# Kernel tuning notes

Measured on AMD Instinct MI355X. Metric: run time of the kernel, lower is better.

Reference implementation:

```python
import jax, jax.numpy as jnp
import numpy as np

T, D, H, E, A = 4096, 1024, 2048, 8, 2


def setup_inputs() -> dict:
    key = jax.random.key(0)
    k1, k2, k3, k4, k5 = jax.random.split(key, 5)
    x = jax.random.normal(k1, (T, D), dtype=jnp.float32)
    expert_indices = jax.random.randint(k2, (T, A), 0, E, dtype=jnp.int64)
    scale = 0.02  # keep activations numerically sane (torch.randn init is unscaled)
    w_gate = jax.random.normal(k3, (E, H, D), dtype=jnp.float32) * scale
    w_up = jax.random.normal(k4, (E, H, D), dtype=jnp.float32) * scale
    w_down = jax.random.normal(k5, (E, D, H), dtype=jnp.float32) * scale
    return {"x": x, "expert_indices": expert_indices,
            "w_gate": w_gate, "w_up": w_up, "w_down": w_down}


def reference(x, expert_indices, w_gate, w_up, w_down):
    # Math identical to: gather per-token expert weights then einsum, but
    # computed as dense all-expert GEMMs + small activation gathers so we
    # never materialize the (T, A, H, D) gathered weight tensors.
    zg = jnp.einsum('td,ehd->teh', x, w_gate)   # (T, E, H)
    zu = jnp.einsum('td,ehd->teh', x, w_up)     # (T, E, H)
    idx = expert_indices[:, :, None]            # (T, A, 1)
    g = jnp.take_along_axis(zg, idx, axis=1)    # (T, A, H)
    u = jnp.take_along_axis(zu, idx, axis=1)    # (T, A, H)
    h = jax.nn.silu(g) * u                      # (T, A, H)
    # Down projection: route h back to its expert with one-hot, dense GEMM.
    oh = jax.nn.one_hot(expert_indices, E, dtype=h.dtype)  # (T, A, E)
    he = jnp.einsum('tah,tae->taeh', h, oh)     # (T, A, E, H)
    out = jnp.einsum('taeh,edh->tad', he, w_down)  # (T, A, D)
    return out
```

## Files before the change

kernel.cpp:

```cpp
#include <hip/hip_runtime.h>

#define NE 8
#define TA 8192
#define MAXT 40
#define MAXPAD (MAXT*256)

typedef __attribute__((ext_vector_type(4)))  float f32x4;
typedef __attribute__((ext_vector_type(16))) float f32x16;
typedef __attribute__((ext_vector_type(8)))  short s16x8;

#define WS_CNT  0
#define WS_CUR  8
#define WS_META 16
#define WS_TEXP 18
#define WS_PERM 256

#define WAITVM0() asm volatile("s_waitcnt vmcnt(0)" ::: "memory")
#define BAR()     asm volatile("s_barrier" ::: "memory")

__device__ __forceinline__ unsigned short f2bf(float f) {
  unsigned u = __builtin_bit_cast(unsigned, f);
  u += 0x7FFFu + ((u >> 16) & 1u);
  return (unsigned short)(u >> 16);
}

__device__ __forceinline__ void glds16(const unsigned short* g, unsigned short* l) {
  __builtin_amdgcn_global_load_lds(
      (const __attribute__((address_space(1))) unsigned int*)g,
      (__attribute__((address_space(3))) unsigned int*)l, 16, 0, 0);
}

template <int STRIDE>
__device__ __forceinline__ void stage_t(const unsigned short* g, unsigned short* Lb,
                                        int k0, int tid) {
#pragma unroll
  for (int i = 0; i < 4; ++i)
    glds16(g + (size_t)i * 64 * STRIDE + k0, Lb + i * 4096 + tid * 8);
}

__global__ void k_count(const int* __restrict__ idx, int* __restrict__ ws) {
  int i = blockIdx.x * 256 + threadIdx.x;
  if (i < TA) atomicAdd(&ws[WS_CNT + idx[i]], 1);
}

__global__ void k_scan(int* __restrict__ ws) {
  if (threadIdx.x == 0) {
    int off = 0, ti = 0;
    for (int e = 0; e < NE; ++e) {
      ws[WS_CUR + e] = off;
      int c = ws[WS_CNT + e];
      int nt = (c + 255) / 256;
      for (int k = 0; k < nt; ++k) ws[WS_TEXP + ti++] = e;
      off += nt * 256;
    }
    ws[WS_META] = ti;
    ws[WS_META + 1] = off;
  }
}

__global__ void k_place(const int* __restrict__ idx, int* __restrict__ ws) {
  int i = blockIdx.x * 256 + threadIdx.x;
  if (i < TA) {
    int e = idx[i];
    int pos = atomicAdd(&ws[WS_CUR + e], 1);
    ws[WS_PERM + pos] = i;
  }
}

__global__ void k_cvt(const float* __restrict__ s, unsigned short* __restrict__ d) {
  int i = (blockIdx.x * 256 + threadIdx.x) * 8;
  f32x4 a = *(const f32x4*)(s + i);
  f32x4 b = *(const f32x4*)(s + i + 4);
  s16x8 o;
  o[0] = (short)f2bf(a[0]); o[1] = (short)f2bf(a[1]);
  o[2] = (short)f2bf(a[2]); o[3] = (short)f2bf(a[3]);
  o[4] = (short)f2bf(b[0]); o[5] = (short)f2bf(b[1]);
  o[6] = (short)f2bf(b[2]); o[7] = (short)f2bf(b[3]);
  *(s16x8*)(d + i) = o;
}

__global__ void k_cvt_gu(const float* __restrict__ s, unsigned short* __restrict__ d, int off) {
  int t = blockIdx.x * 256 + threadIdx.x;
  int i = t * 8;
  int dd = i & 1023;
  int h = (i >> 10) & 2047;
  int e = i >> 21;
  int drow = (e << 12) + ((h >> 5) << 6) + off + (h & 31);
  f32x4 a = *(const f32x4*)(s + i);
  f32x4 b = *(const f32x4*)(s + i + 4);
  s16x8 o;
  o[0] = (short)f2bf(a[0]); o[1] = (short)f2bf(a[1]);
  o[2] = (short)f2bf(a[2]); o[3] = (short)f2bf(a[3]);
  o[4] = (short)f2bf(b[0]); o[5] = (short)f2bf(b[1]);
  o[6] = (short)f2bf(b[2]); o[7] = (short)f2bf(b[3]);
  *(s16x8*)(d + (size_t)drow * 1024 + dd) = o;
}

__global__ void k_gather(const float* __restrict__ x, const int* __restrict__ ws,
                         unsigned short* __restrict__ xb) {
  int tid = blockIdx.x * 256 + threadIdx.x;
  int r = tid >> 7;
  int c = (tid & 127) << 3;
  int ta = ws[WS_PERM + r];
  s16x8 o = {0,0,0,0,0,0,0,0};
  if (ta >= 0) {
    const float* xp = x + (size_t)(ta >> 1) * 1024 + c;
    f32x4 a = *(const f32x4*)xp;
    f32x4 b = *(const f32x4*)(xp + 4);
    o[0] = (short)f2bf(a[0]); o[1] = (short)f2bf(a[1]);
    o[2] = (short)f2bf(a[2]); o[3] = (short)f2bf(a[3]);
    o[4] = (short)f2bf(b[0]); o[5] = (short)f2bf(b[1]);
    o[6] = (short)f2bf(b[2]); o[7] = (short)f2bf(b[3]);
  }
  *(s16x8*)(xb + (size_t)r * 1024 + c) = o;
}

__global__ __launch_bounds__(512) void k_gemm1(
    const unsigned short* __restrict__ xb, const unsigned short* __restrict__ wgu,
    unsigned short* __restrict__ hb, const int* __restrict__ ws) {
  int mt = blockIdx.y;
  if (mt >= ws[WS_META]) return;
  int e = ws[WS_TEXP + mt];
  int nt = blockIdx.x;

  __shared__ unsigned short L[2][32768];

  int tid = threadIdx.x;
  int lane = tid & 63, wid = tid >> 6;
  int wm = wid >> 2, wn = wid & 3;
  int lr = tid >> 3;
  int cs = (tid & 7) ^ (lr & 7);

  const unsigned short* gA = xb  + (size_t)(mt * 256 + lr) * 1024 + cs * 8;
  const unsigned short* gB = wgu + (size_t)(e * 4096 + nt * 256 + lr) * 1024 + cs * 8;

  f32x16 accg[4] = {};
  f32x16 accu[4] = {};

  int r31 = lane & 31, kg = lane >> 5, x7 = r31 & 7;
  int arow = wm * 128 + r31;
  int brow = wn * 64 + r31;

  stage_t<1024>(gA, &L[0][0], 0, tid);
  stage_t<1024>(gB, &L[0][16384], 0, tid);

#pragma unroll 2
  for (int kt = 0; kt < 16; ++kt) {
    int cur = kt & 1;
    WAITVM0();
    BAR();
    if (kt + 1 < 16) {
      stage_t<1024>(gA, &L[cur ^ 1][0],     (kt + 1) * 64, tid);
      stage_t<1024>(gB, &L[cur ^ 1][16384], (kt + 1) * 64, tid);
    }
    const unsigned short* Ab = &L[cur][0];
    const unsigned short* Bb = &L[cur][16384];
#pragma unroll
    for (int ks = 0; ks < 4; ++ks) {
      int kc = ks * 2 + kg;
      int slot = (kc ^ x7) * 8;
      s16x8 a[4], bg, bu;
#pragma unroll
      for (int mi = 0; mi < 4; ++mi)
        a[mi] = *(const s16x8*)&Ab[(arow + mi * 32) * 64 + slot];
      bg = *(const s16x8*)&Bb[brow * 64 + slot];
      bu = *(const s16x8*)&Bb[(brow + 32) * 64 + slot];
      __builtin_amdgcn_s_setprio(1);
#pragma unroll
      for (int mi = 0; mi < 4; ++mi) {
        accg[mi] = __builtin_amdgcn_mfma_f32_32x32x16_bf16(a[mi], bg, accg[mi], 0, 0, 0);
        accu[mi] = __builtin_amdgcn_mfma_f32_32x32x16_bf16(a[mi], bu, accu[mi], 0, 0, 0);
      }
      __builtin_amdgcn_s_setprio(0);
    }
  }

  int hrow0 = mt * 256 + wm * 128;
  int hcol  = nt * 128 + wn * 32 + r31;
#pragma unroll
  for (int mi = 0; mi < 4; ++mi)
#pragma unroll
    for (int r = 0; r < 16; ++r) {
      int crow = (r & 3) + 8 * (r >> 2) + 4 * kg;
      float g = accg[mi][r];
      float u = accu[mi][r];
      float h = (g / (1.f + __expf(-g))) * u;
      hb[(size_t)(hrow0 + mi * 32 + crow) * 2048 + hcol] = f2bf(h);
    }
}

__global__ __launch_bounds__(512) void k_gemm2(
    const unsigned short* __restrict__ hb, const unsigned short* __restrict__ wdb,
    float* __restrict__ out, const int* __restrict__ ws) {
  int mt = blockIdx.y;
  if (mt >= ws[WS_META]) return;
  int e = ws[WS_TEXP + mt];
  int nt = blockIdx.x;

  __shared__ unsigned short L[2][32768];

  int tid = threadIdx.x;
  int lane = tid & 63, wid = tid >> 6;
  int wm = wid >> 2, wn = wid & 3;
  int lr = tid >> 3;
  int cs = (tid & 7) ^ (lr & 7);

  const unsigned short* gA = hb  + (size_t)(mt * 256 + lr) * 2048 + cs * 8;
  const unsigned short* gB = wdb + (size_t)(e * 1024 + nt * 256 + lr) * 2048 + cs * 8;

  f32x16 acc0[4] = {};
  f32x16 acc1[4] = {};

  int r31 = lane & 31, kg = lane >> 5, x7 = r31 & 7;
  int arow = wm * 128 + r31;
  int brow = wn * 64 + r31;

  stage_t<2048>(gA, &L[0][0], 0, tid);
  stage_t<2048>(gB, &L[0][16384], 0, tid);

#pragma unroll 2
  for (int kt = 0; kt < 32; ++kt) {
    int cur = kt & 1;
    WAITVM0();
    BAR();
    if (kt + 1 < 32) {
      stage_t<2048>(gA, &L[cur ^ 1][0],     (kt + 1) * 64, tid);
      stage_t<2048>(gB, &L[cur ^ 1][16384], (kt + 1) * 64, tid);
    }
    const unsigned short* Ab = &L[cur][0];
    const unsigned short* Bb = &L[cur][16384];
#pragma unroll
    for (int ks = 0; ks < 4; ++ks) {
      int kc = ks * 2 + kg;
      int slot = (kc ^ x7) * 8;
      s16x8 a[4], b0, b1;
#pragma unroll
      for (int mi = 0; mi < 4; ++mi)
        a[mi] = *(const s16x8*)&Ab[(arow + mi * 32) * 64 + slot];
      b0 = *(const s16x8*)&Bb[brow * 64 + slot];
      b1 = *(const s16x8*)&Bb[(brow + 32) * 64 + slot];
      __builtin_amdgcn_s_setprio(1);
#pragma unroll
      for (int mi = 0; mi < 4; ++mi) {
        acc0[mi] = __builtin_amdgcn_mfma_f32_32x32x16_bf16(a[mi], b0, acc0[mi], 0, 0, 0);
        acc1[mi] = __builtin_amdgcn_mfma_f32_32x32x16_bf16(a[mi], b1, acc1[mi], 0, 0, 0);
      }
      __builtin_amdgcn_s_setprio(0);
    }
  }

  int prow0 = mt * 256 + wm * 128;
  int dcol  = nt * 256 + wn * 64 + r31;
#pragma unroll
  for (int mi = 0; mi < 4; ++mi)
#pragma unroll
    for (int r = 0; r < 16; ++r) {
      int crow = (r & 3) + 8 * (r >> 2) + 4 * kg;
      int ta = ws[WS_PERM + prow0 + mi * 32 + crow];
      if (ta >= 0) {
        out[(size_t)ta * 1024 + dcol]      = acc0[mi][r];
        out[(size_t)ta * 1024 + dcol + 32] = acc1[mi][r];
      }
    }
}

extern "C" void kernel_launch(void* const* d_in, const int* in_sizes, int n_in,
                              void* d_out, int out_size, void* d_ws, size_t ws_size,
                              hipStream_t stream) {
  const float* x   = (const float*)d_in[0];
  const int*   idx = (const int*)d_in[1];
  const float* wg  = (const float*)d_in[2];
  const float* wu  = (const float*)d_in[3];
  const float* wd  = (const float*)d_in[4];
  float* out = (float*)d_out;

  int*  wsi = (int*)d_ws;
  char* wsb = (char*)d_ws;
  const size_t OFF_XB  = 65536;
  const size_t OFF_WDB = 65536;
  const size_t OFF_WGU = 65536 + (size_t)NE * 1024 * 2048 * 2;
  const size_t OFF_HB  = OFF_WGU + (size_t)NE * 4096 * 1024 * 2;
  unsigned short* xbuf = (unsigned short*)(wsb + OFF_XB);
  unsigned short* wdb  = (unsigned short*)(wsb + OFF_WDB);
  unsigned short* wgu  = (unsigned short*)(wsb + OFF_WGU);
  unsigned short* hb   = (unsigned short*)(wsb + OFF_HB);

  hipMemsetAsync(wsi, 0, 96 * sizeof(int), stream);
  hipMemsetAsync(wsi + WS_PERM, 0xFF, MAXPAD * sizeof(int), stream);

  k_count<<<TA / 256, 256, 0, stream>>>(idx, wsi);
  k_scan<<<1, 64, 0, stream>>>(wsi);
  k_place<<<TA / 256, 256, 0, stream>>>(idx, wsi);

  k_cvt_gu<<<(NE * 2048 * 1024) / (256 * 8), 256, 0, stream>>>(wg, wgu, 0);
  k_cvt_gu<<<(NE * 2048 * 1024) / (256 * 8), 256, 0, stream>>>(wu, wgu, 32);
  k_gather<<<(MAXPAD * 128) / 256, 256, 0, stream>>>(x, wsi, xbuf);

  k_gemm1<<<dim3(16, MAXT), 512, 0, stream>>>(xbuf, wgu, hb, wsi);

  k_cvt<<<(NE * 1024 * 2048) / (256 * 8), 256, 0, stream>>>(wd, wdb);

  k_gemm2<<<dim3(4, MAXT), 512, 0, stream>>>(hb, wdb, out, wsi);
}
```

Before: 317.6 us.

## Fuse routing kernels, merge gate/up conversion, finer-grained pipelining, split-K down GEMM

Replaces the count/scan/place kernels and two memsets with a single-block routing kernel using shared-memory counters. Gate and up weight conversion is merged into one kernel. Both GEMMs now stage K in 32-wide halves with partial vmcnt waits, so the next tile's loads overlap compute at finer granularity. The down GEMM is split in two along K, with atomic float adds into a zeroed output, which doubles its block count at the cost of atomic traffic and a memset.

```diff
diff --git a/kernel.cpp b/kernel.cpp
--- a/kernel.cpp
+++ b/kernel.cpp
@@ -9,13 +9,12 @@
 typedef __attribute__((ext_vector_type(16))) float f32x16;
 typedef __attribute__((ext_vector_type(8)))  short s16x8;
 
-#define WS_CNT  0
 #define WS_CUR  8
 #define WS_META 16
 #define WS_TEXP 18
 #define WS_PERM 256
 
-#define WAITVM0() asm volatile("s_waitcnt vmcnt(0)" ::: "memory")
+#define WAITVM(N) asm volatile("s_waitcnt vmcnt(" #N ")" ::: "memory")
 #define BAR()     asm volatile("s_barrier" ::: "memory")
 
 __device__ __forceinline__ unsigned short f2bf(float f) {
@@ -30,41 +29,60 @@
       (__attribute__((address_space(3))) unsigned int*)l, 16, 0, 0);
 }
 
-template <int STRIDE>
-__device__ __forceinline__ void stage_t(const unsigned short* g, unsigned short* Lb,
-                                        int k0, int tid) {
-#pragma unroll
-  for (int i = 0; i < 4; ++i)
-    glds16(g + (size_t)i * 64 * STRIDE + k0, Lb + i * 4096 + tid * 8);
-}
-
-__global__ void k_count(const int* __restrict__ idx, int* __restrict__ ws) {
-  int i = blockIdx.x * 256 + threadIdx.x;
-  if (i < TA) atomicAdd(&ws[WS_CNT + idx[i]], 1);
-}
-
-__global__ void k_scan(int* __restrict__ ws) {
-  if (threadIdx.x == 0) {
+__global__ void k_route(const int* __restrict__ idx, int* __restrict__ ws) {
+  __shared__ int cnt[NE];
+  int t = threadIdx.x;
+  if (t < NE) cnt[t] = 0;
+  __syncthreads();
+  int e0[8];
+#pragma unroll
+  for (int k = 0; k < 8; ++k) { e0[k] = idx[t + k * 1024]; atomicAdd(&cnt[e0[k]], 1); }
+  __syncthreads();
+  if (t == 0) {
     int off = 0, ti = 0;
     for (int e = 0; e < NE; ++e) {
       ws[WS_CUR + e] = off;
-      int c = ws[WS_CNT + e];
-      int nt = (c + 255) / 256;
-      for (int k = 0; k < nt; ++k) ws[WS_TEXP + ti++] = e;
-      off += nt * 256;
+      int c = cnt[e];
+      int ntl = (c + 255) >> 8;
+      for (int k = 0; k < ntl; ++k) ws[WS_TEXP + ti++] = e;
+      off += ntl << 8;
     }
     ws[WS_META] = ti;
     ws[WS_META + 1] = off;
   }
-}
-
-__global__ void k_place(const int* __restrict__ idx, int* __restrict__ ws) {
-  int i = blockIdx.x * 256 + threadIdx.x;
-  if (i < TA) {
-    int e = idx[i];
-    int pos = atomicAdd(&ws[WS_CUR + e], 1);
-    ws[WS_PERM + pos] = i;
-  }
+#pragma unroll
+  for (int k = 0; k < MAXPAD / 1024; ++k) ws[WS_PERM + t + k * 1024] = -1;
+  __syncthreads();
+#pragma unroll
+  for (int k = 0; k < 8; ++k) {
+    int p = atomicAdd(&ws[WS_CUR + e0[k]], 1);
+    ws[WS_PERM + p] = t + k * 1024;
+  }
+}
+
+__global__ void k_cvt_gu2(const float* __restrict__ g, const float* __restrict__ u,
+                          unsigned short* __restrict__ d) {
+  int t = blockIdx.x * 256 + threadIdx.x;
+  int i = t * 8;
+  int dd = i & 1023;
+  int h = (i >> 10) & 2047;
+  int e = i >> 21;
+  int dr = (e << 12) + ((h >> 5) << 6) + (h & 31);
+  f32x4 a = *(const f32x4*)(g + i);
+  f32x4 b = *(const f32x4*)(g + i + 4);
+  s16x8 o;
+  o[0] = (short)f2bf(a[0]); o[1] = (short)f2bf(a[1]);
+  o[2] = (short)f2bf(a[2]); o[3] = (short)f2bf(a[3]);
+  o[4] = (short)f2bf(b[0]); o[5] = (short)f2bf(b[1]);
+  o[6] = (short)f2bf(b[2]); o[7] = (short)f2bf(b[3]);
+  *(s16x8*)(d + (size_t)dr * 1024 + dd) = o;
+  a = *(const f32x4*)(u + i);
+  b = *(const f32x4*)(u + i + 4);
+  o[0] = (short)f2bf(a[0]); o[1] = (short)f2bf(a[1]);
+  o[2] = (short)f2bf(a[2]); o[3] = (short)f2bf(a[3]);
+  o[4] = (short)f2bf(b[0]); o[5] = (short)f2bf(b[1]);
+  o[6] = (short)f2bf(b[2]); o[7] = (short)f2bf(b[3]);
+  *(s16x8*)(d + (size_t)(dr + 32) * 1024 + dd) = o;
 }
 
 __global__ void k_cvt(const float* __restrict__ s, unsigned short* __restrict__ d) {
@@ -77,23 +95,6 @@
   o[4] = (short)f2bf(b[0]); o[5] = (short)f2bf(b[1]);
   o[6] = (short)f2bf(b[2]); o[7] = (short)f2bf(b[3]);
   *(s16x8*)(d + i) = o;
-}
-
-__global__ void k_cvt_gu(const float* __restrict__ s, unsigned short* __restrict__ d, int off) {
-  int t = blockIdx.x * 256 + threadIdx.x;
-  int i = t * 8;
-  int dd = i & 1023;
-  int h = (i >> 10) & 2047;
-  int e = i >> 21;
-  int drow = (e << 12) + ((h >> 5) << 6) + off + (h & 31);
-  f32x4 a = *(const f32x4*)(s + i);
-  f32x4 b = *(const f32x4*)(s + i + 4);
-  s16x8 o;
-  o[0] = (short)f2bf(a[0]); o[1] = (short)f2bf(a[1]);
-  o[2] = (short)f2bf(a[2]); o[3] = (short)f2bf(a[3]);
-  o[4] = (short)f2bf(b[0]); o[5] = (short)f2bf(b[1]);
-  o[6] = (short)f2bf(b[2]); o[7] = (short)f2bf(b[3]);
-  *(s16x8*)(d + (size_t)drow * 1024 + dd) = o;
 }
 
 __global__ void k_gather(const float* __restrict__ x, const int* __restrict__ ws,
@@ -115,6 +116,17 @@
   *(s16x8*)(xb + (size_t)r * 1024 + c) = o;
 }
 
+
+#define STG(LB, H, K0, RSTEP)                                          \
+  {                                                                    \
+    unsigned short* Ld = (LB) + (H) * 8192 + tid * 8;                  \
+    int ko = (K0) + (H) * 32;                                          \
+    glds16(gAs + ko,           Ld);                                    \
+    glds16(gAs + ko + (RSTEP), Ld + 4096);                             \
+    glds16(gBs + ko,           Ld + 16384);                            \
+    glds16(gBs + ko + (RSTEP), Ld + 16384 + 4096);                     \
+  }
+
 __global__ __launch_bounds__(512) void k_gemm1(
     const unsigned short* __restrict__ xb, const unsigned short* __restrict__ wgu,
     unsigned short* __restrict__ hb, const int* __restrict__ ws) {
@@ -128,52 +140,65 @@
   int tid = threadIdx.x;
   int lane = tid & 63, wid = tid >> 6;
   int wm = wid >> 2, wn = wid & 3;
-  int lr = tid >> 3;
-  int cs = (tid & 7) ^ (lr & 7);
-
-  const unsigned short* gA = xb  + (size_t)(mt * 256 + lr) * 1024 + cs * 8;
-  const unsigned short* gB = wgu + (size_t)(e * 4096 + nt * 256 + lr) * 1024 + cs * 8;
+  int r31 = lane & 31, kg = lane >> 5, x3 = r31 & 3;
+
+  int rl  = tid >> 2;
+  int csw = (tid & 3) ^ (rl & 3);
+
+  const unsigned short* gAs = xb  + (size_t)(mt * 256 + rl) * 1024 + csw * 8;
+  const unsigned short* gBs = wgu + (size_t)(e * 4096 + nt * 256 + rl) * 1024 + csw * 8;
 
   f32x16 accg[4] = {};
   f32x16 accu[4] = {};
 
-  int r31 = lane & 31, kg = lane >> 5, x7 = r31 & 7;
-  int arow = wm * 128 + r31;
-  int brow = wn * 64 + r31;
-
-  stage_t<1024>(gA, &L[0][0], 0, tid);
-  stage_t<1024>(gB, &L[0][16384], 0, tid);
+  int aof0 = (wm * 128 + r31) * 32;
+  int aof1 = aof0 + 1024;
+  int aof2 = aof0 + 2048;
+  int aof3 = aof0 + 3072;
+  int bgo  = (wn * 64 + r31) * 32;
+
+#define CMP1(LC, P)                                                          \
+  {                                                                          \
+    const unsigned short* Ab = (LC) + (P) * 8192;                            \
+    const unsigned short* Bb = Ab + 16384;                                   \
+    _Pragma("unroll")                                                        \
+    for (int ksl = 0; ksl < 2; ++ksl) {                                      \
+      int sc = ((kg + 2 * ksl) ^ x3) << 3;                                   \
+      s16x8 a0 = *(const s16x8*)&Ab[aof0 + sc];                              \
+      s16x8 a1 = *(const s16x8*)&Ab[aof1 + sc];                              \
+      s16x8 a2 = *(const s16x8*)&Ab[aof2 + sc];                              \
+      s16x8 a3 = *(const s16x8*)&Ab[aof3 + sc];                              \
+      s16x8 bg = *(const s16x8*)&Bb[bgo + sc];                               \
+      s16x8 bu = *(const s16x8*)&Bb[bgo + 1024 + sc];                        \
+      __builtin_amdgcn_s_setprio(1);                                         \
+      accg[0] = __builtin_amdgcn_mfma_f32_32x32x16_bf16(a0, bg, accg[0], 0,0,0); \
+      accu[0] = __builtin_amdgcn_mfma_f32_32x32x16_bf16(a0, bu, accu[0], 0,0,0); \
+      accg[1] = __builtin_amdgcn_mfma_f32_32x32x16_bf16(a1, bg, accg[1], 0,0,0); \
+      accu[1] = __builtin_amdgcn_mfma_f32_32x32x16_bf16(a1, bu, accu[1], 0,0,0); \
+      accg[2] = __builtin_amdgcn_mfma_f32_32x32x16_bf16(a2, bg, accg[2], 0,0,0); \
+      accu[2] = __builtin_amdgcn_mfma_f32_32x32x16_bf16(a2, bu, accu[2], 0,0,0); \
+      accg[3] = __builtin_amdgcn_mfma_f32_32x32x16_bf16(a3, bg, accg[3], 0,0,0); \
+      accu[3] = __builtin_amdgcn_mfma_f32_32x32x16_bf16(a3, bu, accu[3], 0,0,0); \
+      __builtin_amdgcn_s_setprio(0);                                         \
+    }                                                                        \
+  }
+
+  STG(&L[0][0], 0, 0, 131072)
+  STG(&L[0][0], 1, 0, 131072)
 
 #pragma unroll 2
   for (int kt = 0; kt < 16; ++kt) {
-    int cur = kt & 1;
-    WAITVM0();
-    BAR();
-    if (kt + 1 < 16) {
-      stage_t<1024>(gA, &L[cur ^ 1][0],     (kt + 1) * 64, tid);
-      stage_t<1024>(gB, &L[cur ^ 1][16384], (kt + 1) * 64, tid);
-    }
-    const unsigned short* Ab = &L[cur][0];
-    const unsigned short* Bb = &L[cur][16384];
-#pragma unroll
-    for (int ks = 0; ks < 4; ++ks) {
-      int kc = ks * 2 + kg;
-      int slot = (kc ^ x7) * 8;
-      s16x8 a[4], bg, bu;
-#pragma unroll
-      for (int mi = 0; mi < 4; ++mi)
-        a[mi] = *(const s16x8*)&Ab[(arow + mi * 32) * 64 + slot];
-      bg = *(const s16x8*)&Bb[brow * 64 + slot];
-      bu = *(const s16x8*)&Bb[(brow + 32) * 64 + slot];
-      __builtin_amdgcn_s_setprio(1);
-#pragma unroll
-      for (int mi = 0; mi < 4; ++mi) {
-        accg[mi] = __builtin_amdgcn_mfma_f32_32x32x16_bf16(a[mi], bg, accg[mi], 0, 0, 0);
-        accu[mi] = __builtin_amdgcn_mfma_f32_32x32x16_bf16(a[mi], bu, accu[mi], 0, 0, 0);
-      }
-      __builtin_amdgcn_s_setprio(0);
-    }
-  }
+    unsigned short* Lc = &L[kt & 1][0];
+    unsigned short* Ln = &L[(kt & 1) ^ 1][0];
+    int kn = (kt + 1 < 16 ? kt + 1 : kt) * 64;
+    WAITVM(4); BAR();
+    STG(Ln, 0, kn, 131072)
+    CMP1(Lc, 0)
+    WAITVM(4); BAR();
+    STG(Ln, 1, kn, 131072)
+    CMP1(Lc, 1)
+  }
+  WAITVM(0);
 
   int hrow0 = mt * 256 + wm * 128;
   int hcol  = nt * 128 + wn * 32 + r31;
@@ -195,59 +220,74 @@
   int mt = blockIdx.y;
   if (mt >= ws[WS_META]) return;
   int e = ws[WS_TEXP + mt];
-  int nt = blockIdx.x;
+  int nt = blockIdx.x & 3;
+  int kslice = blockIdx.x >> 2;
+  int kb = kslice * 1024;
 
   __shared__ unsigned short L[2][32768];
 
   int tid = threadIdx.x;
   int lane = tid & 63, wid = tid >> 6;
   int wm = wid >> 2, wn = wid & 3;
-  int lr = tid >> 3;
-  int cs = (tid & 7) ^ (lr & 7);
-
-  const unsigned short* gA = hb  + (size_t)(mt * 256 + lr) * 2048 + cs * 8;
-  const unsigned short* gB = wdb + (size_t)(e * 1024 + nt * 256 + lr) * 2048 + cs * 8;
+  int r31 = lane & 31, kg = lane >> 5, x3 = r31 & 3;
+
+  int rl  = tid >> 2;
+  int csw = (tid & 3) ^ (rl & 3);
+
+  const unsigned short* gAs = hb  + (size_t)(mt * 256 + rl) * 2048 + kb + csw * 8;
+  const unsigned short* gBs = wdb + (size_t)(e * 1024 + nt * 256 + rl) * 2048 + kb + csw * 8;
 
   f32x16 acc0[4] = {};
   f32x16 acc1[4] = {};
 
-  int r31 = lane & 31, kg = lane >> 5, x7 = r31 & 7;
-  int arow = wm * 128 + r31;
-  int brow = wn * 64 + r31;
-
-  stage_t<2048>(gA, &L[0][0], 0, tid);
-  stage_t<2048>(gB, &L[0][16384], 0, tid);
+  int aof0 = (wm * 128 + r31) * 32;
+  int aof1 = aof0 + 1024;
+  int aof2 = aof0 + 2048;
+  int aof3 = aof0 + 3072;
+  int bgo  = (wn * 64 + r31) * 32;
+
+#define CMP2(LC, P)                                                          \
+  {                                                                          \
+    const unsigned short* Ab = (LC) + (P) * 8192;                            \
+    const unsigned short* Bb = Ab + 16384;                                   \
+    _Pragma("unroll")                                                        \
+    for (int ksl = 0; ksl < 2; ++ksl) {                                      \
+      int sc = ((kg + 2 * ksl) ^ x3) << 3;                                   \
+      s16x8 a0 = *(const s16x8*)&Ab[aof0 + sc];                              \
+      s16x8 a1 = *(const s16x8*)&Ab[aof1 + sc];                              \
+      s16x8 a2 = *(const s16x8*)&Ab[aof2 + sc];                              \
+      s16x8 a3 = *(const s16x8*)&Ab[aof3 + sc];                              \
+      s16x8 b0 = *(const s16x8*)&Bb[bgo + sc];                               \
+      s16x8 b1 = *(const s16x8*)&Bb[bgo + 1024 + sc];                        \
+      __builtin_amdgcn_s_setprio(1);                                         \
+      acc0[0] = __builtin_amdgcn_mfma_f32_32x32x16_bf16(a0, b0, acc0[0], 0,0,0); \
+      acc1[0] = __builtin_amdgcn_mfma_f32_32x32x16_bf16(a0, b1, acc1[0], 0,0,0); \
+      acc0[1] = __builtin_amdgcn_mfma_f32_32x32x16_bf16(a1, b0, acc0[1], 0,0,0); \
+      acc1[1] = __builtin_amdgcn_mfma_f32_32x32x16_bf16(a1, b1, acc1[1], 0,0,0); \
+      acc0[2] = __builtin_amdgcn_mfma_f32_32x32x16_bf16(a2, b0, acc0[2], 0,0,0); \
+      acc1[2] = __builtin_amdgcn_mfma_f32_32x32x16_bf16(a2, b1, acc1[2], 0,0,0); \
+      acc0[3] = __builtin_amdgcn_mfma_f32_32x32x16_bf16(a3, b0, acc0[3], 0,0,0); \
+      acc1[3] = __builtin_amdgcn_mfma_f32_32x32x16_bf16(a3, b1, acc1[3], 0,0,0); \
+      __builtin_amdgcn_s_setprio(0);                                         \
+    }                                                                        \
+  }
+
+  STG(&L[0][0], 0, 0, 262144)
+  STG(&L[0][0], 1, 0, 262144)
 
 #pragma unroll 2
-  for (int kt = 0; kt < 32; ++kt) {
-    int cur = kt & 1;
-    WAITVM0();
-    BAR();
-    if (kt + 1 < 32) {
-      stage_t<2048>(gA, &L[cur ^ 1][0],     (kt + 1) * 64, tid);
-      stage_t<2048>(gB, &L[cur ^ 1][16384], (kt + 1) * 64, tid);
-    }
-    const unsigned short* Ab = &L[cur][0];
-    const unsigned short* Bb = &L[cur][16384];
-#pragma unroll
-    for (int ks = 0; ks < 4; ++ks) {
-      int kc = ks * 2 + kg;
-      int slot = (kc ^ x7) * 8;
-      s16x8 a[4], b0, b1;
-#pragma unroll
-      for (int mi = 0; mi < 4; ++mi)
-        a[mi] = *(const s16x8*)&Ab[(arow + mi * 32) * 64 + slot];
-      b0 = *(const s16x8*)&Bb[brow * 64 + slot];
-      b1 = *(const s16x8*)&Bb[(brow + 32) * 64 + slot];
-      __builtin_amdgcn_s_setprio(1);
-#pragma unroll
-      for (int mi = 0; mi < 4; ++mi) {
-        acc0[mi] = __builtin_amdgcn_mfma_f32_32x32x16_bf16(a[mi], b0, acc0[mi], 0, 0, 0);
-        acc1[mi] = __builtin_amdgcn_mfma_f32_32x32x16_bf16(a[mi], b1, acc1[mi], 0, 0, 0);
-      }
-      __builtin_amdgcn_s_setprio(0);
-    }
-  }
+  for (int kt = 0; kt < 16; ++kt) {
+    unsigned short* Lc = &L[kt & 1][0];
+    unsigned short* Ln = &L[(kt & 1) ^ 1][0];
+    int kn = (kt + 1 < 16 ? kt + 1 : kt) * 64;
+    WAITVM(4); BAR();
+    STG(Ln, 0, kn, 262144)
+    CMP2(Lc, 0)
+    WAITVM(4); BAR();
+    STG(Ln, 1, kn, 262144)
+    CMP2(Lc, 1)
+  }
+  WAITVM(0);
 
   int prow0 = mt * 256 + wm * 128;
   int dcol  = nt * 256 + wn * 64 + r31;
@@ -258,8 +298,8 @@
       int crow = (r & 3) + 8 * (r >> 2) + 4 * kg;
       int ta = ws[WS_PERM + prow0 + mi * 32 + crow];
       if (ta >= 0) {
-        out[(size_t)ta * 1024 + dcol]      = acc0[mi][r];
-        out[(size_t)ta * 1024 + dcol + 32] = acc1[mi][r];
+        unsafeAtomicAdd(&out[(size_t)ta * 1024 + dcol],      acc0[mi][r]);
+        unsafeAtomicAdd(&out[(size_t)ta * 1024 + dcol + 32], acc1[mi][r]);
       }
     }
 }
@@ -285,20 +325,14 @@
   unsigned short* wgu  = (unsigned short*)(wsb + OFF_WGU);
   unsigned short* hb   = (unsigned short*)(wsb + OFF_HB);
 
-  hipMemsetAsync(wsi, 0, 96 * sizeof(int), stream);
-  hipMemsetAsync(wsi + WS_PERM, 0xFF, MAXPAD * sizeof(int), stream);
-
-  k_count<<<TA / 256, 256, 0, stream>>>(idx, wsi);
-  k_scan<<<1, 64, 0, stream>>>(wsi);
-  k_place<<<TA / 256, 256, 0, stream>>>(idx, wsi);
-
-  k_cvt_gu<<<(NE * 2048 * 1024) / (256 * 8), 256, 0, stream>>>(wg, wgu, 0);
-  k_cvt_gu<<<(NE * 2048 * 1024) / (256 * 8), 256, 0, stream>>>(wu, wgu, 32);
+  k_route<<<1, 1024, 0, stream>>>(idx, wsi);
+  k_cvt_gu2<<<(NE * 2048 * 1024) / (256 * 8), 256, 0, stream>>>(wg, wu, wgu);
   k_gather<<<(MAXPAD * 128) / 256, 256, 0, stream>>>(x, wsi, xbuf);
 
   k_gemm1<<<dim3(16, MAXT), 512, 0, stream>>>(xbuf, wgu, hb, wsi);
 
   k_cvt<<<(NE * 1024 * 2048) / (256 * 8), 256, 0, stream>>>(wd, wdb);
 
-  k_gemm2<<<dim3(4, MAXT), 512, 0, stream>>>(hb, wdb, out, wsi);
-}
+  hipMemsetAsync(out, 0, (size_t)out_size * sizeof(float), stream);
+  k_gemm2<<<dim3(8, MAXT), 512, 0, stream>>>(hb, wdb, out, wsi);
+}
```

Measured after the change: 330.3 us. 4.0% more time.
